# Performance work log

Hardware: AMD Instinct MI355X
Metric: run time of the kernel (lower is better)

## Reference

```python
import jax, jax.numpy as jnp
import numpy as np

DIM = 192
HEADS = 8
B, H, W = 8, 128, 128

def _dwconv3x3(x, w):
    # x: [B,C,H,W], w: [C,1,3,3] depthwise
    return jax.lax.conv_general_dilated(
        x, w, window_strides=(1, 1), padding=((1, 1), (1, 1)),
        dimension_numbers=('NCHW', 'OIHW', 'NCHW'),
        feature_group_count=x.shape[1])

def _proj(x, pw, dw):
    # 1x1 pointwise (as einsum) followed by 3x3 depthwise
    y = jnp.einsum('bchw,oc->bohw', x, pw)
    return _dwconv3x3(y, dw)

def setup_inputs() -> dict:
    key = jax.random.key(0)
    ks = jax.random.split(key, 9)
    s_pw = 1.0 / np.sqrt(DIM)
    s_dw = 1.0 / 3.0
    return {
        'x_feat': jax.random.normal(ks[0], (B, DIM, H, W), jnp.float32),
        'y_feat': jax.random.normal(ks[1], (B, DIM, H, W), jnp.float32),
        'q_pw': jax.random.normal(ks[2], (DIM, DIM), jnp.float32) * s_pw,
        'q_dw': jax.random.normal(ks[3], (DIM, 1, 3, 3), jnp.float32) * s_dw,
        'k_pw': jax.random.normal(ks[4], (DIM, DIM), jnp.float32) * s_pw,
        'k_dw': jax.random.normal(ks[5], (DIM, 1, 3, 3), jnp.float32) * s_dw,
        'v_pw': jax.random.normal(ks[6], (DIM, DIM), jnp.float32) * s_pw,
        'v_dw': jax.random.normal(ks[7], (DIM, 1, 3, 3), jnp.float32) * s_dw,
        'proj_w': jax.random.normal(ks[8], (DIM, DIM), jnp.float32) * s_pw,
        'temperature': jnp.ones((HEADS, 1, 1), jnp.float32),
    }

def reference(x_feat, y_feat, q_pw, q_dw, k_pw, k_dw, v_pw, v_dw, proj_w, temperature):
    b, c, h, w = x_feat.shape
    ch = c // HEADS  # channels per head
    q = _proj(x_feat, q_pw, q_dw)
    k = _proj(y_feat, k_pw, k_dw)
    v = _proj(y_feat, v_pw, v_dw)
    # b (head c) h w -> b head c (h w)
    to_heads = lambda t: t.reshape(b, HEADS, ch, h * w)
    q, k, v = to_heads(q), to_heads(k), to_heads(v)
    # L2-normalize along token dim (torch F.normalize eps=1e-12)
    q = q / jnp.maximum(jnp.linalg.norm(q, axis=-1, keepdims=True), 1e-12)
    k = k / jnp.maximum(jnp.linalg.norm(k, axis=-1, keepdims=True), 1e-12)
    attn = jnp.einsum('bhcn,bhdn->bhcd', q, k) * temperature  # [b,heads,ch,ch]
    attn = jax.nn.softmax(attn, axis=-1)
    out = jnp.einsum('bhcd,bhdn->bhcn', attn, v)
    out = out.reshape(b, c, h, w)
    out = jnp.einsum('bchw,oc->bohw', out, proj_w)
    return out
```

## Files before the change

kernel.cpp:

```cpp
#include <hip/hip_runtime.h>
#include <hip/hip_bf16.h>

#define BATCH 8
#define CDIM 192
#define HEADS 8
#define CH 24
#define HH 128
#define WW 128
#define NPIX (HH*WW)
#define NELEM (BATCH*CDIM*NPIX)
#define NP4 (NPIX/4)

#define DSLAB 16
#define NJOBS 624

typedef __attribute__((ext_vector_type(8))) short bf16x8;
typedef __attribute__((ext_vector_type(4))) float f32x4;
typedef __attribute__((ext_vector_type(4))) unsigned int u32x4;
typedef __attribute__((ext_vector_type(8))) unsigned short u16x8;

#define UNIT 100663296ull
__device__ __align__(256) unsigned char g_pool[4 * UNIT + (16u << 20)];

#define OFF_T0   (0 * UNIT)
#define OFF_QB   (1 * UNIT)
#define OFF_KB   (2 * UNIT)
#define OFF_V    (3 * UNIT)
#define OFF_MISC (4 * UNIT)
#define OFF_PART (OFF_MISC)
#define OFF_S    (OFF_MISC + 2555904ull)
#define OFF_M    (OFF_S + 159744ull)
#define OFF_MF   (OFF_M + 1179648ull)

__device__ inline unsigned short bf_rne(float x) {
  unsigned u = __float_as_uint(x);
  unsigned r = (u + 0x7fffu + ((u >> 16) & 1u)) >> 16;
  return (unsigned short)r;
}
__device__ inline void f32_split(float x, unsigned short& h, unsigned short& l) {
  h = bf_rne(x);
  float hf = __uint_as_float(((unsigned)h) << 16);
  l = bf_rne(x - hf);
}

__global__ __launch_bounds__(64) void w_to_frag(const float* __restrict__ W,
                                                unsigned short* __restrict__ F,
                                                int nb) {
  const int b = blockIdx.x / 12, mf = blockIdx.x % 12;
  const int lane = threadIdx.x;
  const int row = mf * 16 + (lane & 15);
  const size_t lo = (size_t)nb * CDIM * CDIM;
#pragma unroll
  for (int ks = 0; ks < 6; ++ks) {
    const int k0 = ks * 32 + (lane >> 4) * 8;
    const float* src = W + ((size_t)b * CDIM + row) * CDIM + k0;
    bf16x8 hv, lv;
#pragma unroll
    for (int j = 0; j < 8; ++j) {
      unsigned short h, l;
      f32_split(src[j], h, l);
      hv[j] = (short)h;
      lv[j] = (short)l;
    }
    const size_t didx = (((size_t)(blockIdx.x) * 6 + ks) * 64 + lane) * 8;
    *(bf16x8*)(F + didx) = hv;
    *(bf16x8*)(F + lo + didx) = lv;
  }
}

__global__ __launch_bounds__(256, 2) void mfma_gemm192(
    const float* __restrict__ X,
    const unsigned short* __restrict__ WF, size_t w_lo,
    int w_bstride,
    float* __restrict__ Out) {
  const int bn = blockIdx.x;
  const int b = blockIdx.y;
  const int t = threadIdx.x;
  const int lane = t & 63, wid = t >> 6;
  const int wm = wid >> 1, wn = wid & 1;
  const int kq = lane >> 4;

  const size_t wbase = (size_t)b * w_bstride;
  const float* Xb = X + (size_t)b * CDIM * NPIX + bn * 64;
  const int pxl = wn * 32 + (lane & 15);

  f32x4 acc[6][2];
#pragma unroll
  for (int mi = 0; mi < 6; ++mi)
#pragma unroll
    for (int ni = 0; ni < 2; ++ni) acc[mi][ni] = (f32x4){0.f, 0.f, 0.f, 0.f};

  for (int ks = 0; ks < 6; ++ks) {
    u32x4 Bh[2], Bl[2];
#pragma unroll
    for (int ni = 0; ni < 2; ++ni) {
      const float* colp = Xb + (size_t)(ks * 32 + kq * 8) * NPIX + pxl + ni * 16;
#pragma unroll
      for (int jp = 0; jp < 4; ++jp) {
        const float x0 = colp[(size_t)(2 * jp) * NPIX];
        const float x1 = colp[(size_t)(2 * jp + 1) * NPIX];
        const unsigned u0 = __float_as_uint(x0);
        const unsigned u1 = __float_as_uint(x1);
        Bh[ni][jp] = (u1 & 0xffff0000u) | (u0 >> 16);
        const float rr0 = x0 - __uint_as_float(u0 & 0xffff0000u);
        const float rr1 = x1 - __uint_as_float(u1 & 0xffff0000u);
        Bl[ni][jp] = ((unsigned)bf_rne(rr1) << 16) | (unsigned)bf_rne(rr0);
      }
    }
    const bf16x8 bh0 = __builtin_bit_cast(bf16x8, Bh[0]);
    const bf16x8 bl0 = __builtin_bit_cast(bf16x8, Bl[0]);
    const bf16x8 bh1 = __builtin_bit_cast(bf16x8, Bh[1]);
    const bf16x8 bl1 = __builtin_bit_cast(bf16x8, Bl[1]);

#pragma unroll
    for (int mi = 0; mi < 6; ++mi) {
      const int mf = wm * 6 + mi;
      const size_t idx = wbase + (((size_t)(mf * 6 + ks)) * 64 + lane) * 8;
      const bf16x8 Ah = *(const bf16x8*)(WF + idx);
      const bf16x8 Al = *(const bf16x8*)(WF + w_lo + idx);
      acc[mi][0] = __builtin_amdgcn_mfma_f32_16x16x32_bf16(Ah, bh0, acc[mi][0], 0, 0, 0);
      acc[mi][0] = __builtin_amdgcn_mfma_f32_16x16x32_bf16(Ah, bl0, acc[mi][0], 0, 0, 0);
      acc[mi][0] = __builtin_amdgcn_mfma_f32_16x16x32_bf16(Al, bh0, acc[mi][0], 0, 0, 0);
      acc[mi][1] = __builtin_amdgcn_mfma_f32_16x16x32_bf16(Ah, bh1, acc[mi][1], 0, 0, 0);
      acc[mi][1] = __builtin_amdgcn_mfma_f32_16x16x32_bf16(Ah, bl1, acc[mi][1], 0, 0, 0);
      acc[mi][1] = __builtin_amdgcn_mfma_f32_16x16x32_bf16(Al, bh1, acc[mi][1], 0, 0, 0);
    }
  }

  const int ocol = bn * 64 + wn * 32 + (lane & 15);
  const int orow = wm * 96 + (lane >> 4) * 4;
#pragma unroll
  for (int mi = 0; mi < 6; ++mi)
#pragma unroll
    for (int r = 0; r < 4; ++r) {
      const int och = orow + mi * 16 + r;
      float* dst = Out + ((size_t)b * CDIM + och) * NPIX + ocol;
      dst[0] = acc[mi][0][r];
      dst[16] = acc[mi][1][r];
    }
}

__global__ __launch_bounds__(256) void dwconv(const float* __restrict__ In,
                                              const float* __restrict__ Wd,
                                              float* __restrict__ Out) {
  const int idx = blockIdx.x * 256 + threadIdx.x;
  const int x8 = (idx & 15) * 8;
  const int y = (idx >> 4) & 127;
  const int c = (idx >> 11) % CDIM;
  const int b = idx / (2048 * CDIM);

  const float* base = In + (size_t)(b * CDIM + c) * NPIX;
  float w[9];
#pragma unroll
  for (int i = 0; i < 9; ++i) w[i] = Wd[c * 9 + i];

  float a[8] = {0.f, 0.f, 0.f, 0.f, 0.f, 0.f, 0.f, 0.f};
#pragma unroll
  for (int dy = 0; dy < 3; ++dy) {
    const int yy = y + dy - 1;
    if (yy < 0 || yy > 127) continue;
    const float* row = base + yy * WW;
    const float lf = (x8 > 0) ? row[x8 - 1] : 0.f;
    const float4 m0 = *(const float4*)(row + x8);
    const float4 m1 = *(const float4*)(row + x8 + 4);
    const float rt = (x8 + 8 < WW) ? row[x8 + 8] : 0.f;
    const float w0 = w[dy * 3 + 0], w1 = w[dy * 3 + 1], w2 = w[dy * 3 + 2];
    a[0] += w0 * lf   + w1 * m0.x + w2 * m0.y;
    a[1] += w0 * m0.x + w1 * m0.y + w2 * m0.z;
    a[2] += w0 * m0.y + w1 * m0.z + w2 * m0.w;
    a[3] += w0 * m0.z + w1 * m0.w + w2 * m1.x;
    a[4] += w0 * m0.w + w1 * m1.x + w2 * m1.y;
    a[5] += w0 * m1.x + w1 * m1.y + w2 * m1.z;
    a[6] += w0 * m1.y + w1 * m1.z + w2 * m1.w;
    a[7] += w0 * m1.z + w1 * m1.w + w2 * rt;
  }
  float4 o0, o1;
  o0.x = a[0]; o0.y = a[1]; o0.z = a[2]; o0.w = a[3];
  o1.x = a[4]; o1.y = a[5]; o1.z = a[6]; o1.w = a[7];
  *(float4*)(Out + (size_t)idx * 8) = o0;
  *(float4*)(Out + (size_t)idx * 8 + 4) = o1;
}

__global__ __launch_bounds__(256) void dwconv_bf(const float* __restrict__ In,
                                                 const float* __restrict__ Wd,
                                                 unsigned short* __restrict__ Out) {
  const int idx = blockIdx.x * 256 + threadIdx.x;
  const int x8 = (idx & 15) * 8;
  const int y = (idx >> 4) & 127;
  const int c = (idx >> 11) % CDIM;
  const int b = idx / (2048 * CDIM);

  const float* base = In + (size_t)(b * CDIM + c) * NPIX;
  float w[9];
#pragma unroll
  for (int i = 0; i < 9; ++i) w[i] = Wd[c * 9 + i];

  float a[8] = {0.f, 0.f, 0.f, 0.f, 0.f, 0.f, 0.f, 0.f};
#pragma unroll
  for (int dy = 0; dy < 3; ++dy) {
    const int yy = y + dy - 1;
    if (yy < 0 || yy > 127) continue;
    const float* row = base + yy * WW;
    const float lf = (x8 > 0) ? row[x8 - 1] : 0.f;
    const float4 m0 = *(const float4*)(row + x8);
    const float4 m1 = *(const float4*)(row + x8 + 4);
    const float rt = (x8 + 8 < WW) ? row[x8 + 8] : 0.f;
    const float w0 = w[dy * 3 + 0], w1 = w[dy * 3 + 1], w2 = w[dy * 3 + 2];
    a[0] += w0 * lf   + w1 * m0.x + w2 * m0.y;
    a[1] += w0 * m0.x + w1 * m0.y + w2 * m0.z;
    a[2] += w0 * m0.y + w1 * m0.z + w2 * m0.w;
    a[3] += w0 * m0.z + w1 * m0.w + w2 * m1.x;
    a[4] += w0 * m0.w + w1 * m1.x + w2 * m1.y;
    a[5] += w0 * m1.x + w1 * m1.y + w2 * m1.z;
    a[6] += w0 * m1.y + w1 * m1.z + w2 * m1.w;
    a[7] += w0 * m1.z + w1 * m1.w + w2 * rt;
  }
  u16x8 hv, lv;
#pragma unroll
  for (int j = 0; j < 8; ++j) {
    unsigned short h, l;
    f32_split(a[j], h, l);
    hv[j] = h;
    lv[j] = l;
  }
  *(u16x8*)(Out + (size_t)idx * 8) = hv;
  *(u16x8*)(Out + NELEM + (size_t)idx * 8) = lv;
}

__global__ __launch_bounds__(256) void dots_mfma(
    const unsigned short* __restrict__ QF,
    const unsigned short* __restrict__ KF,
    float* __restrict__ Part) {
  const int bh = blockIdx.x;
  const int slab = blockIdx.y;
  const int b = bh >> 3, h = bh & 7;
  const int t = threadIdx.x;
  const int lane = t & 63, wid = t >> 6;

  const size_t rowbase = (size_t)(b * CDIM + h * CH);
  const int px0 = slab * 1024 + wid * 256;
  const int rr = lane & 15;
  const int j8 = (lane >> 4) * 8;

  f32x4 accx[2][2], aqq[2], aqhl[2], akk[2], akhl[2];
#pragma unroll
  for (int mi = 0; mi < 2; ++mi) {
#pragma unroll
    for (int ni = 0; ni < 2; ++ni) accx[mi][ni] = (f32x4){0.f, 0.f, 0.f, 0.f};
    aqq[mi] = (f32x4){0.f, 0.f, 0.f, 0.f};
    aqhl[mi] = (f32x4){0.f, 0.f, 0.f, 0.f};
    akk[mi] = (f32x4){0.f, 0.f, 0.f, 0.f};
    akhl[mi] = (f32x4){0.f, 0.f, 0.f, 0.f};
  }

  auto load_step = [&](int s, bf16x8 (&qh)[2], bf16x8 (&ql)[2],
                       bf16x8 (&kh)[2], bf16x8 (&kl)[2]) {
    const int px = px0 + s * 32 + j8;
#pragma unroll
    for (int mi = 0; mi < 2; ++mi) {
      const size_t off = (rowbase + mi * 16 + rr) * (size_t)NPIX + px;
      qh[mi] = *(const bf16x8*)(QF + off);
      ql[mi] = *(const bf16x8*)(QF + NELEM + off);
      kh[mi] = *(const bf16x8*)(KF + off);
      kl[mi] = *(const bf16x8*)(KF + NELEM + off);
    }
  };
  auto mfma_step = [&](bf16x8 (&qh)[2], bf16x8 (&ql)[2], bf16x8 (&kh)[2],
                       bf16x8 (&kl)[2]) {
#pragma unroll
    for (int mi = 0; mi < 2; ++mi) {
#pragma unroll
      for (int ni = 0; ni < 2; ++ni) {
        accx[mi][ni] = __builtin_amdgcn_mfma_f32_16x16x32_bf16(
            qh[mi], kh[ni], accx[mi][ni], 0, 0, 0);
        accx[mi][ni] = __builtin_amdgcn_mfma_f32_16x16x32_bf16(
            qh[mi], kl[ni], accx[mi][ni], 0, 0, 0);
        accx[mi][ni] = __builtin_amdgcn_mfma_f32_16x16x32_bf16(
            ql[mi], kh[ni], accx[mi][ni], 0, 0, 0);
      }
      aqq[mi] = __builtin_amdgcn_mfma_f32_16x16x32_bf16(qh[mi], qh[mi],
                                                        aqq[mi], 0, 0, 0);
      aqhl[mi] = __builtin_amdgcn_mfma_f32_16x16x32_bf16(qh[mi], ql[mi],
                                                         aqhl[mi], 0, 0, 0);
      akk[mi] = __builtin_amdgcn_mfma_f32_16x16x32_bf16(kh[mi], kh[mi],
                                                        akk[mi], 0, 0, 0);
      akhl[mi] = __builtin_amdgcn_mfma_f32_16x16x32_bf16(kh[mi], kl[mi],
                                                         akhl[mi], 0, 0, 0);
    }
  };

  bf16x8 Aqh[2], Aql[2], Akh[2], Akl[2];
  bf16x8 Bqh[2], Bql[2], Bkh[2], Bkl[2];
  load_step(0, Aqh, Aql, Akh, Akl);
#pragma unroll
  for (int s = 0; s < 8; s += 2) {
    if (s + 1 < 8) load_step(s + 1, Bqh, Bql, Bkh, Bkl);
    mfma_step(Aqh, Aql, Akh, Akl);
    if (s + 2 < 8) load_step(s + 2, Aqh, Aql, Akh, Akl);
    mfma_step(Bqh, Bql, Bkh, Bkl);
  }

  __shared__ float xls[4][24][24];
  __shared__ float qls[4][24], kls[4][24];
  const int col = lane & 15;
  const int rbase = (lane >> 4) * 4;
#pragma unroll
  for (int mi = 0; mi < 2; ++mi) {
#pragma unroll
    for (int ni = 0; ni < 2; ++ni) {
      const int d = ni * 16 + col;
      if (d < 24) {
#pragma unroll
        for (int r = 0; r < 4; ++r) {
          const int c = mi * 16 + rbase + r;
          if (c < 24) xls[wid][c][d] = accx[mi][ni][r];
        }
      }
    }
    const int cc = mi * 16 + col;
    const int rd = col - rbase;
    if (cc < 24 && rd >= 0 && rd < 4) {
      qls[wid][cc] = aqq[mi][rd] + 2.f * aqhl[mi][rd];
      kls[wid][cc] = akk[mi][rd] + 2.f * akhl[mi][rd];
    }
  }
  __syncthreads();

  float* P = Part + ((size_t)bh * DSLAB + slab) * NJOBS;
  for (int j = t; j < 576; j += 256) {
    const int c = j / 24, d = j % 24;
    P[j] = xls[0][c][d] + xls[1][c][d] + xls[2][c][d] + xls[3][c][d];
  }
  if (t < 24) P[576 + t] = qls[0][t] + qls[1][t] + qls[2][t] + qls[3][t];
  else if (t >= 32 && t < 56) {
    const int c = t - 32;
    P[600 + c] = kls[0][c] + kls[1][c] + kls[2][c] + kls[3][c];
  }
}

__global__ __launch_bounds__(640) void dots_reduce(const float* __restrict__ Part,
                                                   float* __restrict__ S) {
  const int bh = blockIdx.x;
  const int job = threadIdx.x;
  if (job >= NJOBS) return;
  float s = 0.f;
  for (int i = 0; i < DSLAB; ++i)
    s += Part[((size_t)bh * DSLAB + i) * NJOBS + job];
  S[bh * NJOBS + job] = s;
}

__global__ __launch_bounds__(576) void build_M(const float* __restrict__ S,
                                               const float* __restrict__ PW,
                                               const float* __restrict__ Temp,
                                               float* __restrict__ M) {
  const int b = blockIdx.x, h = blockIdx.y;
  const int bh = b * 8 + h;
  __shared__ float att[CH][CH];
  __shared__ float qn[CH], kn[CH];
  const int t = threadIdx.x;
  const float* Sb = S + (size_t)bh * NJOBS;

  if (t < CH) {
    qn[t] = fmaxf(sqrtf(Sb[576 + t]), 1e-12f);
    kn[t] = fmaxf(sqrtf(Sb[600 + t]), 1e-12f);
  }
  __syncthreads();
  const float temp = Temp[h];
  if (t < 576) {
    const int c = t / 24, d = t % 24;
    att[c][d] = Sb[t] / (qn[c] * kn[d]) * temp;
  }
  __syncthreads();
  if (t < CH) {
    float mx = -1e30f;
    for (int d = 0; d < CH; ++d) mx = fmaxf(mx, att[t][d]);
    float sum = 0.f;
    for (int d = 0; d < CH; ++d) {
      const float e = __expf(att[t][d] - mx);
      att[t][d] = e;
      sum += e;
    }
    const float inv = 1.f / sum;
    for (int d = 0; d < CH; ++d) att[t][d] *= inv;
  }
  __syncthreads();
  for (int i = t; i < CDIM * CH; i += 576) {
    const int o = i / CH, d = i % CH;
    float s = 0.f;
#pragma unroll
    for (int c = 0; c < CH; ++c) s += PW[o * CDIM + h * CH + c] * att[c][d];
    M[((size_t)b * CDIM + o) * CDIM + h * CH + d] = s;
  }
}


extern "C" void kernel_launch(void* const* d_in, const int* in_sizes, int n_in,
                              void* d_out, int out_size, void* d_ws, size_t ws_size,
                              hipStream_t stream) {
  const float* x_feat = (const float*)d_in[0];
  const float* y_feat = (const float*)d_in[1];
  const float* q_pw   = (const float*)d_in[2];
  const float* q_dw   = (const float*)d_in[3];
  const float* k_pw   = (const float*)d_in[4];
  const float* k_dw   = (const float*)d_in[5];
  const float* v_pw   = (const float*)d_in[6];
  const float* v_dw   = (const float*)d_in[7];
  const float* proj_w = (const float*)d_in[8];
  const float* temp   = (const float*)d_in[9];
  float* out = (float*)d_out;

  unsigned char* pool;
  (void)hipGetSymbolAddress((void**)&pool, HIP_SYMBOL(g_pool));
  float* t0 = (float*)(pool + OFF_T0);
  unsigned short* QB = (unsigned short*)(pool + OFF_QB);
  unsigned short* KB = (unsigned short*)(pool + OFF_KB);
  float* v  = (float*)(pool + OFF_V);
  float* part = (float*)(pool + OFF_PART);
  float* S    = (float*)(pool + OFF_S);
  float* M    = (float*)(pool + OFF_M);
  unsigned short* MF = (unsigned short*)(pool + OFF_MF);

  unsigned short* WQF = MF + 2ull * 8 * CDIM * CDIM;
  unsigned short* WKF = WQF + 2ull * CDIM * CDIM;
  unsigned short* WVF = WKF + 2ull * CDIM * CDIM;

  const size_t w1_lo = (size_t)1 * CDIM * CDIM;
  const size_t w8_lo = (size_t)8 * CDIM * CDIM;

  const dim3 ggrid(NPIX / 64, BATCH);
  const int dwgrid = (NELEM / 8) / 256;

  w_to_frag<<<12, 64, 0, stream>>>(q_pw, WQF, 1);
  w_to_frag<<<12, 64, 0, stream>>>(k_pw, WKF, 1);
  w_to_frag<<<12, 64, 0, stream>>>(v_pw, WVF, 1);

  mfma_gemm192<<<ggrid, 256, 0, stream>>>(x_feat, WQF, w1_lo, 0, t0);
  dwconv_bf<<<dwgrid, 256, 0, stream>>>(t0, q_dw, QB);
  mfma_gemm192<<<ggrid, 256, 0, stream>>>(y_feat, WKF, w1_lo, 0, t0);
  dwconv_bf<<<dwgrid, 256, 0, stream>>>(t0, k_dw, KB);

  dots_mfma<<<dim3(64, DSLAB), 256, 0, stream>>>(QB, KB, part);
  dots_reduce<<<64, 640, 0, stream>>>(part, S);
  build_M<<<dim3(BATCH, HEADS), 576, 0, stream>>>(S, proj_w, temp, M);
  w_to_frag<<<8 * 12, 64, 0, stream>>>(M, MF, 8);

  mfma_gemm192<<<ggrid, 256, 0, stream>>>(y_feat, WVF, w1_lo, 0, t0);
  dwconv<<<dwgrid, 256, 0, stream>>>(t0, v_dw, v);

  mfma_gemm192<<<ggrid, 256, 0, stream>>>(v, MF, w8_lo, CDIM * CDIM, out);
}
```

Before: 501.5 us.

## Stage X tile through LDS and give each wave all 192 output rows

The GEMM kernel now loads each 32-row K slab of the input tile into shared memory with coalesced float4 loads (XOR-swizzled to avoid bank conflicts), and each wave reads its B fragment from LDS. The wave partition changes from 2x2 (96 rows x 32 pixels) to 1x4 (all 192 rows x 16 pixels), so each pixel column is split into bf16 hi/lo once instead of twice across waves. This removes strided scalar global loads and duplicated conversion work. In exchange it adds two barriers per K step and makes every wave load all weight fragments, which doubles weight traffic per block.

Result: slower. 547.3 us (+9.1%).

```diff
diff --git a/kernel.cpp b/kernel.cpp
--- a/kernel.cpp
+++ b/kernel.cpp
@@ -76,67 +76,63 @@
   const int bn = blockIdx.x;
   const int b = blockIdx.y;
   const int t = threadIdx.x;
-  const int lane = t & 63, wid = t >> 6;
-  const int wm = wid >> 1, wn = wid & 1;
+  const int lane = t & 63, wn = t >> 6;
   const int kq = lane >> 4;
+
+  __shared__ float Xs[32][68];
 
   const size_t wbase = (size_t)b * w_bstride;
   const float* Xb = X + (size_t)b * CDIM * NPIX + bn * 64;
-  const int pxl = wn * 32 + (lane & 15);
-
-  f32x4 acc[6][2];
-#pragma unroll
-  for (int mi = 0; mi < 6; ++mi)
-#pragma unroll
-    for (int ni = 0; ni < 2; ++ni) acc[mi][ni] = (f32x4){0.f, 0.f, 0.f, 0.f};
+  const int col = (wn * 16 + (lane & 15)) ^ ((kq >> 1) << 4);
+  const int r0 = t >> 4;
+  const int col4 = (t & 15) * 4;
+
+  f32x4 acc[12];
+#pragma unroll
+  for (int mi = 0; mi < 12; ++mi) acc[mi] = (f32x4){0.f, 0.f, 0.f, 0.f};
 
   for (int ks = 0; ks < 6; ++ks) {
-    u32x4 Bh[2], Bl[2];
-#pragma unroll
-    for (int ni = 0; ni < 2; ++ni) {
-      const float* colp = Xb + (size_t)(ks * 32 + kq * 8) * NPIX + pxl + ni * 16;
-#pragma unroll
-      for (int jp = 0; jp < 4; ++jp) {
-        const float x0 = colp[(size_t)(2 * jp) * NPIX];
-        const float x1 = colp[(size_t)(2 * jp + 1) * NPIX];
-        const unsigned u0 = __float_as_uint(x0);
-        const unsigned u1 = __float_as_uint(x1);
-        Bh[ni][jp] = (u1 & 0xffff0000u) | (u0 >> 16);
-        const float rr0 = x0 - __uint_as_float(u0 & 0xffff0000u);
-        const float rr1 = x1 - __uint_as_float(u1 & 0xffff0000u);
-        Bl[ni][jp] = ((unsigned)bf_rne(rr1) << 16) | (unsigned)bf_rne(rr0);
-      }
-    }
-    const bf16x8 bh0 = __builtin_bit_cast(bf16x8, Bh[0]);
-    const bf16x8 bl0 = __builtin_bit_cast(bf16x8, Bl[0]);
-    const bf16x8 bh1 = __builtin_bit_cast(bf16x8, Bh[1]);
-    const bf16x8 bl1 = __builtin_bit_cast(bf16x8, Bl[1]);
-
-#pragma unroll
-    for (int mi = 0; mi < 6; ++mi) {
-      const int mf = wm * 6 + mi;
-      const size_t idx = wbase + (((size_t)(mf * 6 + ks)) * 64 + lane) * 8;
+    float4 s0 = *(const float4*)(Xb + (size_t)(ks * 32 + r0) * NPIX + col4);
+    float4 s1 = *(const float4*)(Xb + (size_t)(ks * 32 + r0 + 16) * NPIX + col4);
+    *(float4*)&Xs[r0][col4] = s0;
+    *(float4*)&Xs[r0 + 16][col4 ^ 16] = s1;
+    __syncthreads();
+
+    u32x4 Bh, Bl;
+#pragma unroll
+    for (int jp = 0; jp < 4; ++jp) {
+      const float x0 = Xs[kq * 8 + 2 * jp][col];
+      const float x1 = Xs[kq * 8 + 2 * jp + 1][col];
+      const unsigned u0 = __float_as_uint(x0);
+      const unsigned u1 = __float_as_uint(x1);
+      Bh[jp] = (u1 & 0xffff0000u) | (u0 >> 16);
+      const float rr0 = x0 - __uint_as_float(u0 & 0xffff0000u);
+      const float rr1 = x1 - __uint_as_float(u1 & 0xffff0000u);
+      Bl[jp] = ((unsigned)bf_rne(rr1) << 16) | (unsigned)bf_rne(rr0);
+    }
+    __syncthreads();
+    const bf16x8 bh = __builtin_bit_cast(bf16x8, Bh);
+    const bf16x8 bl = __builtin_bit_cast(bf16x8, Bl);
+
+#pragma unroll
+    for (int mi = 0; mi < 12; ++mi) {
+      const size_t idx = wbase + (((size_t)(mi * 6 + ks)) * 64 + lane) * 8;
       const bf16x8 Ah = *(const bf16x8*)(WF + idx);
       const bf16x8 Al = *(const bf16x8*)(WF + w_lo + idx);
-      acc[mi][0] = __builtin_amdgcn_mfma_f32_16x16x32_bf16(Ah, bh0, acc[mi][0], 0, 0, 0);
-      acc[mi][0] = __builtin_amdgcn_mfma_f32_16x16x32_bf16(Ah, bl0, acc[mi][0], 0, 0, 0);
-      acc[mi][0] = __builtin_amdgcn_mfma_f32_16x16x32_bf16(Al, bh0, acc[mi][0], 0, 0, 0);
-      acc[mi][1] = __builtin_amdgcn_mfma_f32_16x16x32_bf16(Ah, bh1, acc[mi][1], 0, 0, 0);
-      acc[mi][1] = __builtin_amdgcn_mfma_f32_16x16x32_bf16(Ah, bl1, acc[mi][1], 0, 0, 0);
-      acc[mi][1] = __builtin_amdgcn_mfma_f32_16x16x32_bf16(Al, bh1, acc[mi][1], 0, 0, 0);
-    }
-  }
-
-  const int ocol = bn * 64 + wn * 32 + (lane & 15);
-  const int orow = wm * 96 + (lane >> 4) * 4;
-#pragma unroll
-  for (int mi = 0; mi < 6; ++mi)
+      acc[mi] = __builtin_amdgcn_mfma_f32_16x16x32_bf16(Ah, bh, acc[mi], 0, 0, 0);
+      acc[mi] = __builtin_amdgcn_mfma_f32_16x16x32_bf16(Ah, bl, acc[mi], 0, 0, 0);
+      acc[mi] = __builtin_amdgcn_mfma_f32_16x16x32_bf16(Al, bh, acc[mi], 0, 0, 0);
+    }
+  }
+
+  const int ocol = bn * 64 + wn * 16 + (lane & 15);
+  const int orow = (lane >> 4) * 4;
+#pragma unroll
+  for (int mi = 0; mi < 12; ++mi)
 #pragma unroll
     for (int r = 0; r < 4; ++r) {
-      const int och = orow + mi * 16 + r;
-      float* dst = Out + ((size_t)b * CDIM + och) * NPIX + ocol;
-      dst[0] = acc[mi][0][r];
-      dst[16] = acc[mi][1][r];
+      const int och = mi * 16 + orow + r;
+      Out[((size_t)b * CDIM + och) * NPIX + ocol] = acc[mi][r];
     }
 }
 
```
